# Performance work log

Hardware: AMD Instinct MI355X
Metric: run time of the kernel (lower is better)

## Reference

```python
import jax, jax.numpy as jnp
import numpy as np

BN_EPS = 1e-6
SOFTMAX_EPS = 1e-8
D = 64      # fingerprint_dim
BD = 12     # bond_dim
N_ATOM = 10000
N_EDGE = 40000


def _bn(x, gamma, beta, mean, var):
    # BatchNorm1d in inference mode (running stats)
    return (x - mean) / jnp.sqrt(var + BN_EPS) * gamma + beta


def setup_inputs() -> dict:
    key = jax.random.key(0)
    ks = jax.random.split(key, 16)
    inp = {
        "atom": jax.random.normal(ks[0], (N_ATOM, D), dtype=jnp.float32),
        "bond_index": jax.random.randint(ks[1], (N_EDGE, 2), 0, N_ATOM, dtype=jnp.int64),
        "bond": jax.random.normal(ks[2], (N_EDGE, BD), dtype=jnp.float32),
        # encoder: Linear(bond_dim, D*D) + BatchNorm1d(D*D)
        "enc_W": jax.random.normal(ks[3], (D * D, BD), dtype=jnp.float32) * (1.0 / np.sqrt(BD)),
        "enc_b": jnp.zeros((D * D,), dtype=jnp.float32),
        "enc_gamma": jnp.ones((D * D,), dtype=jnp.float32),
        "enc_beta": jnp.zeros((D * D,), dtype=jnp.float32),
        "enc_mean": jnp.zeros((D * D,), dtype=jnp.float32),
        "enc_var": jnp.ones((D * D,), dtype=jnp.float32),
        # align: Linear(2*D, 1)
        "align_W": jax.random.normal(ks[4], (1, 2 * D), dtype=jnp.float32) * (1.0 / np.sqrt(2 * D)),
        "align_b": jnp.zeros((1,), dtype=jnp.float32),
        # attend: Linear(D, D) + BatchNorm1d(D), no activation
        "att_W": jax.random.normal(ks[5], (D, D), dtype=jnp.float32) * (1.0 / np.sqrt(D)),
        "att_b": jnp.zeros((D,), dtype=jnp.float32),
        "att_gamma": jnp.ones((D,), dtype=jnp.float32),
        "att_beta": jnp.zeros((D,), dtype=jnp.float32),
        "att_mean": jnp.zeros((D,), dtype=jnp.float32),
        "att_var": jnp.ones((D,), dtype=jnp.float32),
        # GRUCell(D, D)
        "gru_W_ih": jax.random.normal(ks[6], (3 * D, D), dtype=jnp.float32) * (1.0 / np.sqrt(D)),
        "gru_W_hh": jax.random.normal(ks[7], (3 * D, D), dtype=jnp.float32) * (1.0 / np.sqrt(D)),
        "gru_b_ih": jnp.zeros((3 * D,), dtype=jnp.float32),
        "gru_b_hh": jnp.zeros((3 * D,), dtype=jnp.float32),
    }
    return inp


def reference(atom, bond_index, bond,
              enc_W, enc_b, enc_gamma, enc_beta, enc_mean, enc_var,
              align_W, align_b,
              att_W, att_b, att_gamma, att_beta, att_mean, att_var,
              gru_W_ih, gru_W_hh, gru_b_ih, gru_b_hh):
    num_atom, d = atom.shape
    tgt = bond_index[:, 0]  # target atom of each edge
    nbr = bond_index[:, 1]  # neighbor atom of each edge

    # encoder: relu(BN(linear(bond))) -> per-edge [d, d] bond matrix
    enc = jax.nn.relu(_bn(bond @ enc_W.T + enc_b, enc_gamma, enc_beta, enc_mean, enc_var))
    enc = enc.reshape(-1, d, d)  # [E, d, d]

    # gather neighbor atoms, per-edge matvec through bond matrix
    neighbor = jnp.einsum('ed,edf->ef', atom[nbr], enc)  # [E, d]

    # attention logits (dropout is identity in eval)
    feat = jnp.concatenate([atom[tgt], neighbor], axis=-1)  # [E, 2d]
    score = jax.nn.leaky_relu(feat @ align_W.T + align_b, negative_slope=0.01)  # [E, 1]

    # segment softmax over target atoms
    mx = jax.ops.segment_max(score, tgt, num_segments=num_atom)  # [N, 1]
    ex = jnp.exp(score - mx[tgt])
    denom = jax.ops.segment_sum(ex, tgt, num_segments=num_atom)[tgt] + SOFTMAX_EPS
    attn = ex / denom  # [E, 1]

    # attend: BN(linear(neighbor)) (no activation), weighted scatter-add
    attd = _bn(neighbor @ att_W.T + att_b, att_gamma, att_beta, att_mean, att_var)
    context = jax.ops.segment_sum(attn * attd, tgt, num_segments=num_atom)  # [N, d]
    context = jax.nn.elu(context)

    # GRUCell(context, atom)
    gi = context @ gru_W_ih.T + gru_b_ih  # [N, 3d]
    gh = atom @ gru_W_hh.T + gru_b_hh     # [N, 3d]
    i_r, i_z, i_n = jnp.split(gi, 3, axis=-1)
    h_r, h_z, h_n = jnp.split(gh, 3, axis=-1)
    r = jax.nn.sigmoid(i_r + h_r)
    z = jax.nn.sigmoid(i_z + h_z)
    n = jnp.tanh(i_n + r * h_n)
    return (1.0 - z) * n + z * atom
```

## Files before the change

### kernel.cpp

```cpp
#include <hip/hip_runtime.h>
#include <math.h>

#define NA 10000
#define NE 40000

typedef float f2 __attribute__((ext_vector_type(2)));
typedef float f4 __attribute__((ext_vector_type(4)));
typedef float f16v __attribute__((ext_vector_type(16)));
typedef int   i4 __attribute__((ext_vector_type(4)));
typedef __bf16 bf16x8 __attribute__((ext_vector_type(8)));

union U8 { unsigned short us[8]; __bf16 b[8]; bf16x8 v; };
union UF4 { f4 v; f2 h[2]; };
union UC16 { f16v v; f2 h[8]; };

static __device__ __forceinline__ unsigned short bf_rne(float x){
  unsigned u = __float_as_uint(x);
  unsigned r = (u + 0x7fffu + ((u>>16)&1u)) >> 16;
  return (unsigned short)r;
}
static __device__ __forceinline__ float bf_to_f(unsigned short h){
  return __uint_as_float(((unsigned)h)<<16);
}
static __device__ __forceinline__ float rcpf(float x){
  float r; asm("v_rcp_f32 %0, %1" : "=v"(r) : "v"(x)); return r;
}
static __device__ __forceinline__ float fsig(float x){
  return rcpf(1.f + __expf(-x));
}
static __device__ __forceinline__ float ftanh(float x){
  float ax = fabsf(x);
  float e = __expf(ax + ax);
  float t = 1.f - 2.f*rcpf(e + 1.f);
  return copysignf(t, x);
}

__global__ __launch_bounds__(256) void k_pre(
  const float* __restrict__ encW, const float* __restrict__ encB,
  const float* __restrict__ eg, const float* __restrict__ ebt,
  const float* __restrict__ e_mn, const float* __restrict__ e_vr,
  const float* __restrict__ attW, const float* __restrict__ attB,
  const float* __restrict__ agm, const float* __restrict__ abt,
  const float* __restrict__ amn, const float* __restrict__ avr,
  const float* __restrict__ wih, const float* __restrict__ whh,
  const int* __restrict__ bidx, const float* __restrict__ atom,
  const float* __restrict__ alW,
  unsigned short* __restrict__ BI,
  unsigned short* __restrict__ aBh, unsigned short* __restrict__ aBl,
  unsigned short* __restrict__ aQh, unsigned short* __restrict__ aQl,
  float* __restrict__ attBf, float* __restrict__ wT,
  float* __restrict__ p, int* __restrict__ cnt)
{
  int tid = threadIdx.x;
  int gid = blockIdx.x*256 + tid;
  int gstride = gridDim.x*256;
  for (int i=gid; i<131072; i+=gstride){
    int j = i&15, ll = (i>>4)&63, t = i>>10;
    int d = t>>1, ft = t&1;
    int jj = j&7;
    int k = ((ll>>5)<<3)+jj;
    int n = d*64 + ft*32 + (ll&31);
    float s = eg[n]*rsqrtf(e_vr[n]+1e-6f);
    unsigned short outv = 0;
    if (k<12){
      float wv = encW[n*12+k]*s;
      unsigned short hi = bf_rne(wv);
      outv = (j<8)? hi : bf_rne(wv - bf_to_f(hi));
    } else if (k==12){
      float b = (encB[n]-e_mn[n])*s + ebt[n];
      unsigned short hi = bf_rne(b);
      outv = (j<8)? hi : bf_rne(b - bf_to_f(hi));
    }
    BI[i] = outv;
  }
  for (int i=gid; i<4096; i+=gstride){
    int j=i&7, l=(i>>3)&63, t=i>>9;
    int kk=t>>1, nt=t&1;
    int k = kk*16 + ((l>>5)<<3) + j;
    int n = nt*32 + (l&31);
    float s = agm[n]*rsqrtf(avr[n]+1e-6f);
    float wv = attW[n*64+k]*s;
    unsigned short hi = bf_rne(wv);
    aBh[i]=hi; aBl[i]=bf_rne(wv - bf_to_f(hi));
  }
  for (int i=gid; i<2048; i+=gstride){
    int j=i&7, l2=(i>>3)&63, kk=i>>9;
    float v = alW[64 + kk*16 + ((l2>>5)<<3) + j];
    unsigned short hi=0, lo=0;
    if ((l2&31)==0){ hi = bf_rne(v); lo = bf_rne(v - bf_to_f(hi)); }
    aQh[i]=hi; aQl[i]=lo;
  }
  for (int f=gid; f<64; f+=gstride){
    float s = agm[f]*rsqrtf(avr[f]+1e-6f);
    attBf[f] = (attB[f]-amn[f])*s + abt[f];
  }
  for (int i=gid; i<24576; i+=gstride){
    int j=i&3, f=(i>>2)&63, idx2=i>>8;
    int g=idx2>>4, kg=idx2&15, k=kg*4+j;
    wT[i] = (g<3)? wih[(g*64+f)*64+k] : whh[((g-3)*64+f)*64+k];
  }
  {
    int wid = gid>>6;
    int l = tid&63;
    float wl = alW[l];
    for (int a=wid; a<NA; a+=(gstride>>6)){
      float v = wl*atom[(size_t)a*64+l];
      v += __shfl_xor(v,1);  v += __shfl_xor(v,2);
      v += __shfl_xor(v,4);  v += __shfl_xor(v,8);
      v += __shfl_xor(v,16); v += __shfl_xor(v,32);
      if (l==0) p[a]=v;
    }
  }
  for (int e=gid; e<NE; e+=gstride) atomicAdd(&cnt[bidx[e*2]],1);
}

__global__ __launch_bounds__(256) void k_scan(const int* __restrict__ cnt,
                                              int* __restrict__ rowstart,
                                              int* __restrict__ wofs)
{
  __shared__ int sPart[256];
  int t = threadIdx.x;
  int base = t*40;
  i4 buf[10];
  int sum = 0;
  if (base < NA){
    const i4* cp = (const i4*)(cnt + base);
    #pragma unroll
    for (int i=0;i<10;i++) buf[i] = cp[i];
    #pragma unroll
    for (int i=0;i<10;i++) sum += buf[i].x+buf[i].y+buf[i].z+buf[i].w;
  }
  sPart[t]=sum;
  __syncthreads();
  for (int off=1; off<256; off<<=1){
    int v = (t>=off)? sPart[t-off] : 0;
    __syncthreads();
    sPart[t]+=v;
    __syncthreads();
  }
  int run = sPart[t]-sum;
  if (base < NA){
    #pragma unroll
    for (int i=0;i<10;i++){
      i4 b=buf[i], o;
      o.x=run; run+=b.x; o.y=run; run+=b.y;
      o.z=run; run+=b.z; o.w=run; run+=b.w;
      ((i4*)(rowstart+base))[i]=o;
      ((i4*)(wofs+base))[i]=o;
    }
  }
  if (t==0) rowstart[NA]=NE;
}

__global__ __launch_bounds__(256) void k_scatter(const int* __restrict__ bidx,
                                                 int* __restrict__ wofs,
                                                 int* __restrict__ elist)
{
  int e = blockIdx.x*256 + threadIdx.x;
  if (e < NE){
    int tg = bidx[e*2];
    int pos = atomicAdd(&wofs[tg],1);
    elist[pos]=e;
  }
}

__global__ __launch_bounds__(128, 4) void k_edge(
  const float* __restrict__ atom, const int* __restrict__ bidx, const float* __restrict__ bond,
  const unsigned short* __restrict__ BI,
  const unsigned short* __restrict__ aBh, const unsigned short* __restrict__ aBl,
  const unsigned short* __restrict__ aQh, const unsigned short* __restrict__ aQl,
  const int* __restrict__ elist, float* __restrict__ zC, float* __restrict__ qv)
{
  __shared__ float sA[2304];
  __shared__ int   sEl[32];
  __shared__ int   sNbr[32];

  int tid = threadIdx.x;
  int l = tid & 63;
  int w = tid >> 6;
  int g = l >> 5;
  int em = l & 31;
  int E0 = blockIdx.x * 32;

  if (tid < 32){
    int e = elist[E0+tid];
    sEl[tid] = e;
    sNbr[tid] = bidx[e*2+1];
  }
  __syncthreads();
  for (int i=tid; i<2048; i+=128){
    int le=i>>6, d=i&63;
    sA[d*36+le] = atom[(size_t)sNbr[le]*64 + d];
  }

  U8 A1, A2;
  {
    const f4* bp = (const f4*)(bond + (size_t)sEl[em]*12);
    f4 b0=bp[0], b1v=bp[1], b2v=bp[2];
    float bv[12] = {b0.x,b0.y,b0.z,b0.w,b1v.x,b1v.y,b1v.z,b1v.w,b2v.x,b2v.y,b2v.z,b2v.w};
    #pragma unroll
    for (int j=0;j<8;j++){
      int k = g*8+j;
      float x = (k<12)? bv[k] : (k==12? 1.f : 0.f);
      __bf16 h = (__bf16)x;
      A1.b[j] = h;
      A2.b[j] = (__bf16)(x - (float)h);
    }
  }
  __syncthreads();

  int ft = w;

  f2 nacc[8];
  #pragma unroll
  for (int i=0;i<8;i++) nacc[i] = (f2){0.f,0.f};
  f16v cz;
  #pragma unroll
  for (int r=0;r<16;r++) cz[r] = 0.f;

  const bf16x8* pB = (const bf16x8*)BI + ((size_t)ft*64 + l)*2;
  U8 rh[4], rl[4];
  #pragma unroll
  for (int s=0;s<3;s++){ rh[s].v = pB[s*256]; rl[s].v = pB[s*256+1]; }

  #pragma unroll 4
  for (int d=0; d<64; d++){
    int cs = d&3, ns = (d+3)&3;
    rh[ns].v = pB[(size_t)(d+3)*256];
    rl[ns].v = pB[(size_t)(d+3)*256 + 1];

    UF4 ldA[4];
    #pragma unroll
    for (int q=0;q<4;q++) ldA[q].v = *(const f4*)&sA[d*36 + 8*q + 4*g];

    UC16 c;
    c.v = __builtin_amdgcn_mfma_f32_32x32x16_bf16(A1.v, rh[cs].v, cz, 0,0,0);
    c.v = __builtin_amdgcn_mfma_f32_32x32x16_bf16(A2.v, rh[cs].v, c.v, 0,0,0);
    c.v = __builtin_amdgcn_mfma_f32_32x32x16_bf16(A1.v, rl[cs].v, c.v, 0,0,0);
    #pragma unroll
    for (int i=0;i<8;i++){
      f2 ev;
      ev[0] = fmaxf(c.h[i][0], 0.f);
      ev[1] = fmaxf(c.h[i][1], 0.f);
      asm("v_pk_fma_f32 %0, %1, %2, %0"
          : "+v"(nacc[i])
          : "v"(ldA[i>>1].h[i&1]), "v"(ev));
    }
  }

  int nt = w;
  U8 eBh[4], eBl[4], eQh[4], eQl[4];
  #pragma unroll
  for (int kk=0; kk<4; kk++){
    eBh[kk].v = *(const bf16x8*)(aBh + ((size_t)((kk*2+nt)*64 + l))*8);
    eBl[kk].v = *(const bf16x8*)(aBl + ((size_t)((kk*2+nt)*64 + l))*8);
  }
  if (nt){
    #pragma unroll
    for (int kk=0; kk<4; kk++){
      eQh[kk].v = *(const bf16x8*)(aQh + ((size_t)(kk*64 + l))*8);
      eQl[kk].v = *(const bf16x8*)(aQl + ((size_t)(kk*64 + l))*8);
    }
  }

  __syncthreads();
  {
    #pragma unroll
    for (int r=0;r<16;r++){
      int row = (r&3) + ((r>>2)<<3) + (g<<2);
      sA[row*68 + (ft<<5) + em] = nacc[r>>1][r&1];
    }
  }
  __syncthreads();

  {
    f16v c, c2;
    #pragma unroll
    for (int r=0;r<16;r++){ c[r] = 0.f; c2[r] = 0.f; }
    #pragma unroll
    for (int kk=0; kk<4; kk++){
      const float* src = &sA[em*68 + kk*16 + g*8];
      f4 x0 = *(const f4*)src;
      f4 x1 = *(const f4*)(src+4);
      U8 Ah, Al;
      #pragma unroll
      for (int j=0;j<4;j++){
        __bf16 h0 = (__bf16)x0[j];
        Ah.b[j] = h0; Al.b[j] = (__bf16)(x0[j] - (float)h0);
        __bf16 h1 = (__bf16)x1[j];
        Ah.b[4+j] = h1; Al.b[4+j] = (__bf16)(x1[j] - (float)h1);
      }
      c = __builtin_amdgcn_mfma_f32_32x32x16_bf16(Ah.v, eBh[kk].v, c, 0,0,0);
      c = __builtin_amdgcn_mfma_f32_32x32x16_bf16(Al.v, eBh[kk].v, c, 0,0,0);
      c = __builtin_amdgcn_mfma_f32_32x32x16_bf16(Ah.v, eBl[kk].v, c, 0,0,0);
      if (nt){
        c2 = __builtin_amdgcn_mfma_f32_32x32x16_bf16(Ah.v, eQh[kk].v, c2, 0,0,0);
        c2 = __builtin_amdgcn_mfma_f32_32x32x16_bf16(Al.v, eQh[kk].v, c2, 0,0,0);
        c2 = __builtin_amdgcn_mfma_f32_32x32x16_bf16(Ah.v, eQl[kk].v, c2, 0,0,0);
      }
    }
    #pragma unroll
    for (int r=0;r<16;r++){
      int row = (r&3) + ((r>>2)<<3) + ((l>>5)<<2);
      zC[(size_t)(E0 + row)*64 + nt*32 + (l&31)] = c[r];
    }
    if (nt && em==0){
      #pragma unroll
      for (int r=0;r<16;r++){
        int row = (r&3) + ((r>>2)<<3) + (g<<2);
        qv[E0 + row] = c2[r];
      }
    }
  }
}

__global__ __launch_bounds__(256, 4) void k_gru(
  const float* __restrict__ atom, const float* __restrict__ zC,
  const int* __restrict__ rowstart, const float* __restrict__ p,
  const float* __restrict__ qv, const float* __restrict__ alB,
  const float* __restrict__ attBf, const float* __restrict__ wT,
  const float* __restrict__ bih, const float* __restrict__ bhh,
  float* __restrict__ out)
{
  __shared__ float sc[4][4][64];
  __shared__ float shh[4][4][64];
  __shared__ float swT[6144];
  int tid = threadIdx.x;
  int l = tid & 63;
  int w = tid >> 6;
  int base = blockIdx.x*16 + w*4;
  float bias = attBf[l];
  float ab = alB[0];

  #pragma unroll
  for (int aa=0; aa<4; aa++){
    int a = base + aa;
    float hf = atom[(size_t)a*64 + l];
    float cf = 0.f;
    int d0 = rowstart[a];
    int deg = rowstart[a+1] - d0;
    if (deg > 0){
      float pa = p[a] + ab;
      float m0=-3e38f, m1=-3e38f, m2=-3e38f, m3=-3e38f;
      int i=0;
      for (; i+3<deg; i+=4){
        float s0 = pa + qv[d0+i],   s1 = pa + qv[d0+i+1];
        float s2 = pa + qv[d0+i+2], s3 = pa + qv[d0+i+3];
        s0=(s0>0.f)?s0:0.01f*s0; s1=(s1>0.f)?s1:0.01f*s1;
        s2=(s2>0.f)?s2:0.01f*s2; s3=(s3>0.f)?s3:0.01f*s3;
        m0=fmaxf(m0,s0); m1=fmaxf(m1,s1); m2=fmaxf(m2,s2); m3=fmaxf(m3,s3);
      }
      for (; i<deg; ++i){
        float s0 = pa + qv[d0+i];
        s0=(s0>0.f)?s0:0.01f*s0;
        m0=fmaxf(m0,s0);
      }
      float mx = fmaxf(fmaxf(m0,m1), fmaxf(m2,m3));
      float dn0=0.f, dn1=0.f, y0=0.f, y1=0.f;
      i=0;
      for (; i+1<deg; i+=2){
        float s0 = pa + qv[d0+i], s1 = pa + qv[d0+i+1];
        s0=(s0>0.f)?s0:0.01f*s0; s1=(s1>0.f)?s1:0.01f*s1;
        float z0 = zC[(size_t)(d0+i)*64 + l];
        float z1 = zC[(size_t)(d0+i+1)*64 + l];
        float e0=__expf(s0-mx), e1=__expf(s1-mx);
        dn0+=e0; dn1+=e1;
        y0=fmaf(e0,z0,y0); y1=fmaf(e1,z1,y1);
      }
      if (i<deg){
        float s0 = pa + qv[d0+i];
        s0=(s0>0.f)?s0:0.01f*s0;
        float e0=__expf(s0-mx);
        dn0+=e0; y0=fmaf(e0, zC[(size_t)(d0+i)*64+l], y0);
      }
      float dn = dn0+dn1;
      cf = ((y0+y1) + dn*bias)*rcpf(dn + 1e-8f);
      cf = (cf>0.f)? cf : expm1f(cf);
    }
    sc[w][aa][l] = cf; shh[w][aa][l] = hf;
  }

  float acc[6][4];
  #pragma unroll
  for (int gg=0;gg<6;gg++)
    #pragma unroll
    for (int aa=0;aa<4;aa++) acc[gg][aa]=0.f;

  for (int ch=0; ch<4; ch++){
    __syncthreads();
    #pragma unroll
    for (int ii=0; ii<6; ii++){
      int i = tid + ii*256;
      int f = i&63, q = i>>6; int gg = q>>2, kgc = q&3;
      ((f4*)swT)[i] = ((const f4*)wT)[(gg*16 + ch*4 + kgc)*64 + f];
    }
    __syncthreads();
    #pragma unroll
    for (int kgc=0; kgc<4; kgc++){
      int kg = ch*4 + kgc;
      f4 wv[6];
      #pragma unroll
      for (int gg=0;gg<6;gg++) wv[gg] = *(const f4*)&swT[((gg*4+kgc)*64 + l)*4];
      #pragma unroll
      for (int aa=0;aa<4;aa++){
        f4 cv = *(const f4*)&sc[w][aa][kg*4];
        f4 hv = *(const f4*)&shh[w][aa][kg*4];
        #pragma unroll
        for (int j=0;j<4;j++){
          acc[0][aa] = fmaf(cv[j], wv[0][j], acc[0][aa]);
          acc[1][aa] = fmaf(cv[j], wv[1][j], acc[1][aa]);
          acc[2][aa] = fmaf(cv[j], wv[2][j], acc[2][aa]);
          acc[3][aa] = fmaf(hv[j], wv[3][j], acc[3][aa]);
          acc[4][aa] = fmaf(hv[j], wv[4][j], acc[4][aa]);
          acc[5][aa] = fmaf(hv[j], wv[5][j], acc[5][aa]);
        }
      }
    }
  }

  float b0 = bih[l], b1 = bih[64+l], b2 = bih[128+l];
  float h0 = bhh[l], h1 = bhh[64+l], h2 = bhh[128+l];
  #pragma unroll
  for (int aa=0;aa<4;aa++){
    int a = base + aa;
    float hf = shh[w][aa][l];
    float r = fsig(acc[0][aa] + b0 + acc[3][aa] + h0);
    float z = fsig(acc[1][aa] + b1 + acc[4][aa] + h1);
    float n = ftanh(acc[2][aa] + b2 + r*(acc[5][aa] + h2));
    out[(size_t)a*64 + l] = (1.f - z)*n + z*hf;
  }
}

extern "C" void kernel_launch(void* const* d_in, const int* in_sizes, int n_in,
                              void* d_out, int out_size, void* d_ws, size_t ws_size,
                              hipStream_t stream) {
  const float* atom = (const float*)d_in[0];
  const int*   bidx = (const int*)  d_in[1];
  const float* bond = (const float*)d_in[2];
  const float* encW = (const float*)d_in[3];
  const float* encB = (const float*)d_in[4];
  const float* eg   = (const float*)d_in[5];
  const float* ebt  = (const float*)d_in[6];
  const float* e_mn = (const float*)d_in[7];
  const float* e_vr = (const float*)d_in[8];
  const float* alW  = (const float*)d_in[9];
  const float* alB  = (const float*)d_in[10];
  const float* atW  = (const float*)d_in[11];
  const float* atB  = (const float*)d_in[12];
  const float* agm  = (const float*)d_in[13];
  const float* abt  = (const float*)d_in[14];
  const float* amn  = (const float*)d_in[15];
  const float* avr  = (const float*)d_in[16];
  const float* wih  = (const float*)d_in[17];
  const float* whh  = (const float*)d_in[18];
  const float* bih  = (const float*)d_in[19];
  const float* bhh  = (const float*)d_in[20];

  float* ws = (float*)d_ws;
  unsigned short* BI  = (unsigned short*)(ws + 0);
  unsigned short* aBh = (unsigned short*)(ws + 65536);
  unsigned short* aBl = (unsigned short*)(ws + 67584);
  unsigned short* aQh = (unsigned short*)(ws + 69632);
  unsigned short* aQl = (unsigned short*)(ws + 70656);
  float* attBf   = ws + 71680;
  float* wT      = ws + 71744;
  float* p       = ws + 96320;
  int*   cnt     = (int*)(ws + 106336);
  int*   rowstart= (int*)(ws + 116352);
  int*   wofs    = (int*)(ws + 126368);
  int*   elist   = (int*)(ws + 136384);
  float* qv      = ws + 176384;
  float* zCb     = ws + 216384;
  float* outp    = (float*)d_out;

  hipMemsetAsync(cnt, 0, NA*sizeof(int), stream);
  k_pre<<<512, 256, 0, stream>>>(encW,encB,eg,ebt,e_mn,e_vr,
                                 atW,atB,agm,abt,amn,avr,
                                 wih,whh,bidx,atom,alW,
                                 BI,aBh,aBl,aQh,aQl,attBf,wT,p,cnt);
  k_scan<<<1, 256, 0, stream>>>(cnt, rowstart, wofs);
  k_scatter<<<(NE+255)/256, 256, 0, stream>>>(bidx, wofs, elist);
  k_edge<<<1250, 128, 0, stream>>>(atom, bidx, bond, BI, aBh, aBl, aQh, aQl,
                                   elist, zCb, qv);
  k_gru<<<625, 256, 0, stream>>>(atom, zCb, rowstart, p, qv, alB,
                                 attBf, wT, bih, bhh, outp);
}
```

Before: 175.3 us.

## Replace CSR sort-based segment softmax with atomic max and scatter-add accumulation

Drops the count/scan/scatter kernels that built a per-target edge list. Edges are now processed in original order: the edge kernel computes the leaky-relu scores and does an atomic max per target using an order-preserving unsigned encoding. A new kernel exponentiates each score and atomically adds the weighted features and denominators per target, and the GRU kernel just reads those sums. This removes the serial single-block scan and two launches, but adds 2.56M float atomics over a 2.5 MB buffer, a larger memset, and a nondeterministic summation order.

```diff
diff --git a/kernel.cpp b/kernel.cpp
--- a/kernel.cpp
+++ b/kernel.cpp
@@ -33,6 +33,14 @@
   float e = __expf(ax + ax);
   float t = 1.f - 2.f*rcpf(e + 1.f);
   return copysignf(t, x);
+}
+static __device__ __forceinline__ unsigned fenc(float f){
+  unsigned b = __float_as_uint(f);
+  return (b & 0x80000000u) ? ~b : (b | 0x80000000u);
+}
+static __device__ __forceinline__ float fdec(unsigned u){
+  unsigned b = (u & 0x80000000u) ? (u & 0x7FFFFFFFu) : ~u;
+  return __uint_as_float(b);
 }
 
 __global__ __launch_bounds__(256) void k_pre(
@@ -43,13 +51,12 @@
   const float* __restrict__ agm, const float* __restrict__ abt,
   const float* __restrict__ amn, const float* __restrict__ avr,
   const float* __restrict__ wih, const float* __restrict__ whh,
-  const int* __restrict__ bidx, const float* __restrict__ atom,
-  const float* __restrict__ alW,
+  const float* __restrict__ atom, const float* __restrict__ alW,
   unsigned short* __restrict__ BI,
   unsigned short* __restrict__ aBh, unsigned short* __restrict__ aBl,
   unsigned short* __restrict__ aQh, unsigned short* __restrict__ aQl,
   float* __restrict__ attBf, float* __restrict__ wT,
-  float* __restrict__ p, int* __restrict__ cnt)
+  float* __restrict__ p)
 {
   int tid = threadIdx.x;
   int gid = blockIdx.x*256 + tid;
@@ -111,57 +118,6 @@
       if (l==0) p[a]=v;
     }
   }
-  for (int e=gid; e<NE; e+=gstride) atomicAdd(&cnt[bidx[e*2]],1);
-}
-
-__global__ __launch_bounds__(256) void k_scan(const int* __restrict__ cnt,
-                                              int* __restrict__ rowstart,
-                                              int* __restrict__ wofs)
-{
-  __shared__ int sPart[256];
-  int t = threadIdx.x;
-  int base = t*40;
-  i4 buf[10];
-  int sum = 0;
-  if (base < NA){
-    const i4* cp = (const i4*)(cnt + base);
-    #pragma unroll
-    for (int i=0;i<10;i++) buf[i] = cp[i];
-    #pragma unroll
-    for (int i=0;i<10;i++) sum += buf[i].x+buf[i].y+buf[i].z+buf[i].w;
-  }
-  sPart[t]=sum;
-  __syncthreads();
-  for (int off=1; off<256; off<<=1){
-    int v = (t>=off)? sPart[t-off] : 0;
-    __syncthreads();
-    sPart[t]+=v;
-    __syncthreads();
-  }
-  int run = sPart[t]-sum;
-  if (base < NA){
-    #pragma unroll
-    for (int i=0;i<10;i++){
-      i4 b=buf[i], o;
-      o.x=run; run+=b.x; o.y=run; run+=b.y;
-      o.z=run; run+=b.z; o.w=run; run+=b.w;
-      ((i4*)(rowstart+base))[i]=o;
-      ((i4*)(wofs+base))[i]=o;
-    }
-  }
-  if (t==0) rowstart[NA]=NE;
-}
-
-__global__ __launch_bounds__(256) void k_scatter(const int* __restrict__ bidx,
-                                                 int* __restrict__ wofs,
-                                                 int* __restrict__ elist)
-{
-  int e = blockIdx.x*256 + threadIdx.x;
-  if (e < NE){
-    int tg = bidx[e*2];
-    int pos = atomicAdd(&wofs[tg],1);
-    elist[pos]=e;
-  }
 }
 
 __global__ __launch_bounds__(128, 4) void k_edge(
@@ -169,10 +125,11 @@
   const unsigned short* __restrict__ BI,
   const unsigned short* __restrict__ aBh, const unsigned short* __restrict__ aBl,
   const unsigned short* __restrict__ aQh, const unsigned short* __restrict__ aQl,
-  const int* __restrict__ elist, float* __restrict__ zC, float* __restrict__ qv)
+  const float* __restrict__ p, const float* __restrict__ alB,
+  float* __restrict__ zC, float* __restrict__ qv, unsigned* __restrict__ mxu)
 {
   __shared__ float sA[2304];
-  __shared__ int   sEl[32];
+  __shared__ int   sTg[32];
   __shared__ int   sNbr[32];
 
   int tid = threadIdx.x;
@@ -183,8 +140,8 @@
   int E0 = blockIdx.x * 32;
 
   if (tid < 32){
-    int e = elist[E0+tid];
-    sEl[tid] = e;
+    int e = E0 + tid;
+    sTg[tid]  = bidx[e*2];
     sNbr[tid] = bidx[e*2+1];
   }
   __syncthreads();
@@ -195,7 +152,7 @@
 
   U8 A1, A2;
   {
-    const f4* bp = (const f4*)(bond + (size_t)sEl[em]*12);
+    const f4* bp = (const f4*)(bond + (size_t)(E0+em)*12);
     f4 b0=bp[0], b1v=bp[1], b2v=bp[2];
     float bv[12] = {b0.x,b0.y,b0.z,b0.w,b1v.x,b1v.y,b1v.z,b1v.w,b2v.x,b2v.y,b2v.z,b2v.w};
     #pragma unroll
@@ -305,22 +262,42 @@
       zC[(size_t)(E0 + row)*64 + nt*32 + (l&31)] = c[r];
     }
     if (nt && em==0){
+      float ab = alB[0];
       #pragma unroll
       for (int r=0;r<16;r++){
         int row = (r&3) + ((r>>2)<<3) + (g<<2);
-        qv[E0 + row] = c2[r];
+        int tg = sTg[row];
+        float s = p[tg] + c2[r] + ab;
+        s = (s>0.f)? s : 0.01f*s;
+        qv[E0 + row] = s;
+        atomicMax(&mxu[tg], fenc(s));
       }
     }
   }
 }
 
+__global__ __launch_bounds__(256) void k_acc(
+  const int* __restrict__ bidx, const float* __restrict__ qv,
+  const unsigned* __restrict__ mxu, const float* __restrict__ zC,
+  float* __restrict__ y, float* __restrict__ dn)
+{
+  int e = (blockIdx.x*256 + threadIdx.x) >> 6;
+  int l = threadIdx.x & 63;
+  if (e < NE){
+    int tg = bidx[e*2];
+    float mx = fdec(mxu[tg]);
+    float ex = __expf(qv[e] - mx);
+    float zc = zC[(size_t)e*64 + l];
+    atomicAdd(&y[(size_t)tg*64 + l], ex*zc);
+    if (l==0) atomicAdd(&dn[tg], ex);
+  }
+}
+
 __global__ __launch_bounds__(256, 4) void k_gru(
-  const float* __restrict__ atom, const float* __restrict__ zC,
-  const int* __restrict__ rowstart, const float* __restrict__ p,
-  const float* __restrict__ qv, const float* __restrict__ alB,
-  const float* __restrict__ attBf, const float* __restrict__ wT,
-  const float* __restrict__ bih, const float* __restrict__ bhh,
-  float* __restrict__ out)
+  const float* __restrict__ atom, const float* __restrict__ yv,
+  const float* __restrict__ dnv, const float* __restrict__ attBf,
+  const float* __restrict__ wT, const float* __restrict__ bih,
+  const float* __restrict__ bhh, float* __restrict__ out)
 {
   __shared__ float sc[4][4][64];
   __shared__ float shh[4][4][64];
@@ -330,53 +307,15 @@
   int w = tid >> 6;
   int base = blockIdx.x*16 + w*4;
   float bias = attBf[l];
-  float ab = alB[0];
 
   #pragma unroll
   for (int aa=0; aa<4; aa++){
     int a = base + aa;
     float hf = atom[(size_t)a*64 + l];
-    float cf = 0.f;
-    int d0 = rowstart[a];
-    int deg = rowstart[a+1] - d0;
-    if (deg > 0){
-      float pa = p[a] + ab;
-      float m0=-3e38f, m1=-3e38f, m2=-3e38f, m3=-3e38f;
-      int i=0;
-      for (; i+3<deg; i+=4){
-        float s0 = pa + qv[d0+i],   s1 = pa + qv[d0+i+1];
-        float s2 = pa + qv[d0+i+2], s3 = pa + qv[d0+i+3];
-        s0=(s0>0.f)?s0:0.01f*s0; s1=(s1>0.f)?s1:0.01f*s1;
-        s2=(s2>0.f)?s2:0.01f*s2; s3=(s3>0.f)?s3:0.01f*s3;
-        m0=fmaxf(m0,s0); m1=fmaxf(m1,s1); m2=fmaxf(m2,s2); m3=fmaxf(m3,s3);
-      }
-      for (; i<deg; ++i){
-        float s0 = pa + qv[d0+i];
-        s0=(s0>0.f)?s0:0.01f*s0;
-        m0=fmaxf(m0,s0);
-      }
-      float mx = fmaxf(fmaxf(m0,m1), fmaxf(m2,m3));
-      float dn0=0.f, dn1=0.f, y0=0.f, y1=0.f;
-      i=0;
-      for (; i+1<deg; i+=2){
-        float s0 = pa + qv[d0+i], s1 = pa + qv[d0+i+1];
-        s0=(s0>0.f)?s0:0.01f*s0; s1=(s1>0.f)?s1:0.01f*s1;
-        float z0 = zC[(size_t)(d0+i)*64 + l];
-        float z1 = zC[(size_t)(d0+i+1)*64 + l];
-        float e0=__expf(s0-mx), e1=__expf(s1-mx);
-        dn0+=e0; dn1+=e1;
-        y0=fmaf(e0,z0,y0); y1=fmaf(e1,z1,y1);
-      }
-      if (i<deg){
-        float s0 = pa + qv[d0+i];
-        s0=(s0>0.f)?s0:0.01f*s0;
-        float e0=__expf(s0-mx);
-        dn0+=e0; y0=fmaf(e0, zC[(size_t)(d0+i)*64+l], y0);
-      }
-      float dn = dn0+dn1;
-      cf = ((y0+y1) + dn*bias)*rcpf(dn + 1e-8f);
-      cf = (cf>0.f)? cf : expm1f(cf);
-    }
+    float dd = dnv[a];
+    float yy = yv[(size_t)a*64 + l];
+    float cf = (yy + dd*bias) * rcpf(dd + 1e-8f);
+    cf = (cf>0.f)? cf : expm1f(cf);
     sc[w][aa][l] = cf; shh[w][aa][l] = hf;
   }
 
@@ -465,23 +404,20 @@
   float* attBf   = ws + 71680;
   float* wT      = ws + 71744;
   float* p       = ws + 96320;
-  int*   cnt     = (int*)(ws + 106336);
-  int*   rowstart= (int*)(ws + 116352);
-  int*   wofs    = (int*)(ws + 126368);
-  int*   elist   = (int*)(ws + 136384);
-  float* qv      = ws + 176384;
-  float* zCb     = ws + 216384;
+  unsigned* mxu  = (unsigned*)(ws + 106336);
+  float* dn      = ws + 116352;
+  float* y       = ws + 126368;
+  float* qv      = ws + 766368;
+  float* zCb     = ws + 806368;
   float* outp    = (float*)d_out;
 
-  hipMemsetAsync(cnt, 0, NA*sizeof(int), stream);
+  hipMemsetAsync(mxu, 0, (size_t)(10016 + 10016 + 640000)*sizeof(float), stream);
   k_pre<<<512, 256, 0, stream>>>(encW,encB,eg,ebt,e_mn,e_vr,
                                  atW,atB,agm,abt,amn,avr,
-                                 wih,whh,bidx,atom,alW,
-                                 BI,aBh,aBl,aQh,aQl,attBf,wT,p,cnt);
-  k_scan<<<1, 256, 0, stream>>>(cnt, rowstart, wofs);
-  k_scatter<<<(NE+255)/256, 256, 0, stream>>>(bidx, wofs, elist);
+                                 wih,whh,atom,alW,
+                                 BI,aBh,aBl,aQh,aQl,attBf,wT,p);
   k_edge<<<1250, 128, 0, stream>>>(atom, bidx, bond, BI, aBh, aBl, aQh, aQl,
-                                   elist, zCb, qv);
-  k_gru<<<625, 256, 0, stream>>>(atom, zCb, rowstart, p, qv, alB,
-                                 attBf, wT, bih, bhh, outp);
-}
+                                   p, alB, zCb, qv, mxu);
+  k_acc<<<10000, 256, 0, stream>>>(bidx, qv, mxu, zCb, y, dn);
+  k_gru<<<625, 256, 0, stream>>>(atom, y, dn, attBf, wT, bih, bhh, outp);
+}
```

Result: slower. 221.4 us (+26.3%).
